# Kernel tuning notes

Hardware: AMD Instinct MI355X
Metric: run time of the kernel (lower is better)

Reference implementation:

```python
import jax, jax.numpy as jnp
import numpy as np

B, T, QD, KD, AD = 64, 2048, 512, 512, 512
SCALING = 1.0
NEG = -1e10


def setup_inputs() -> dict:
    key = jax.random.key(0)
    ks = jax.random.split(key, 10)
    s = 0.02
    return {
        "query": jax.random.normal(ks[0], (B, QD), jnp.float32),
        "keys": jax.random.normal(ks[1], (B, T, KD), jnp.float32),
        "value": jax.random.normal(ks[2], (B, T, KD), jnp.float32),
        "cover": jax.random.uniform(ks[3], (B, T), jnp.float32),
        "key_len": jax.random.randint(ks[4], (B,), T // 2, T + 1),
        "Wq": jax.random.normal(ks[5], (QD, AD), jnp.float32) * s,
        "bq": jnp.zeros((AD,), jnp.float32),
        "Wk": jax.random.normal(ks[6], (KD, AD), jnp.float32) * s,
        "Wc": jax.random.normal(ks[7], (1, AD), jnp.float32) * s,
        "Wo": jax.random.normal(ks[8], (AD, 1), jnp.float32) * s,
    }


def reference(query, keys, value, cover, key_len, Wq, bq, Wk, Wc, Wo):
    # projections
    q = query @ Wq + bq                      # [B, A]
    k = jnp.einsum("btd,da->bta", keys, Wk)  # [B, T, A]
    c = cover[..., None] * Wc[0]             # [B, T, A]  (Linear(1, A), no bias)
    # additive energy
    e = jnp.tanh(q[:, None, :] + k + c)      # [B, T, A]
    energy = jnp.einsum("bta,ao->bot", e, Wo)  # [B, 1, T]
    # mask padded positions (t >= key_len)
    mask = jnp.arange(T)[None, None, :] >= key_len[:, None, None]  # [B, 1, T]
    energy = jnp.where(mask, NEG, energy)
    attn = jax.nn.softmax(energy * SCALING, axis=2)  # [B, 1, T]
    context = jnp.einsum("bqt,btd->bqd", attn, value)[:, 0, :]  # [B, KD]
    return context, attn
```

## Files before the change

kernel.cpp:

```cpp
#include <hip/hip_runtime.h>
#include <hip/hip_bf16.h>

#define B_ 64
#define T_ 2048
#define D_ 512
#define A_ 512
#define BM 128
#define BN 128
#define BK 32
#define NSTEP (D_/BK)

typedef float f32x4_t __attribute__((ext_vector_type(4)));
typedef short bf16x8_t __attribute__((ext_vector_type(8)));

#define GLL16(g, l) __builtin_amdgcn_global_load_lds( \
    (const __attribute__((address_space(1))) void*)(g), \
    (__attribute__((address_space(3))) void*)(l), 16, 0, 0)

__global__ void __launch_bounds__(256) qproj_kernel(
    const float* __restrict__ query, const float* __restrict__ Wq,
    const float* __restrict__ bq, float* __restrict__ qbuf) {
  __shared__ float qs[D_];
  const int b = blockIdx.x, tid = threadIdx.x;
  qs[tid] = query[b*D_ + tid];
  qs[tid+256] = query[b*D_ + tid + 256];
  __syncthreads();
  float a0 = bq[tid], a1 = bq[tid+256];
  for (int d = 0; d < D_; ++d) {
    const float qv = qs[d];
    a0 += qv * Wq[d*A_ + tid];
    a1 += qv * Wq[d*A_ + tid + 256];
  }
  qbuf[b*A_ + tid] = a0;
  qbuf[b*A_ + tid+256] = a1;
}

__global__ void __launch_bounds__(256) wkprep_kernel(
    const float* __restrict__ Wk, unsigned int* __restrict__ slab) {
  __shared__ float tile[32][65];
  const int kb = blockIdx.x >> 3;
  const int a0 = (blockIdx.x & 7) * 64;
  const int tid = threadIdx.x;
  for (int p = 0; p < 8; ++p) {
    const int idx = p*256 + tid;
    const int k = idx >> 6, al = idx & 63;
    tile[k][al] = Wk[(kb*32 + k)*A_ + a0 + al];
  }
  __syncthreads();
  const int al = tid >> 2, c = tid & 3;
  const int a = a0 + al;
  union { __hip_bfloat162 h[2]; uint2 u; } w0, w1;
  w0.h[0] = __float22bfloat162_rn(make_float2(tile[c*8+0][al], tile[c*8+1][al]));
  w0.h[1] = __float22bfloat162_rn(make_float2(tile[c*8+2][al], tile[c*8+3][al]));
  w1.h[0] = __float22bfloat162_rn(make_float2(tile[c*8+4][al], tile[c*8+5][al]));
  w1.h[1] = __float22bfloat162_rn(make_float2(tile[c*8+6][al], tile[c*8+7][al]));
  const int cpos = c ^ ((a >> 1) & 3);
  *(uint4*)(slab + (kb*512 + a)*16 + cpos*4) =
      make_uint4(w0.u.x, w0.u.y, w1.u.x, w1.u.y);
}

__global__ void __launch_bounds__(256, 3) energy_kernel(
    const float* __restrict__ keys, const float* __restrict__ cover,
    const int* __restrict__ key_len, const unsigned char* __restrict__ slab,
    const float* __restrict__ qbuf, const float* __restrict__ Wc,
    const float* __restrict__ Wo, float* __restrict__ epart) {
  __shared__ __align__(16) float Afp[2][BM*BK];
  __shared__ __align__(16) unsigned char Bbuf[2][BN*64];
  __shared__ float redbuf[4][64];

  const int d = blockIdx.x;
  const int logical = (d & 7) * 512 + (d >> 3);
  const int ct = logical & 3;
  const int tt = (logical >> 2) & 15;
  const int b  = logical >> 6;

  const int t0 = tt * BM;
  const int kl = key_len[b];
  if (t0 >= kl) return;

  const int tid = threadIdx.x;
  const int wid = tid >> 6;
  const int lane = tid & 63;
  const int lq = lane >> 4, lr = lane & 15;
  const int wm = wid >> 1, wn = wid & 1;

  const int lrow = lane >> 3;
  const int lchunk = (lane & 7) ^ lrow;
  const float* agA[4];
  #pragma unroll
  for (int j = 0; j < 4; ++j) {
    const int r = (wid*4 + j)*8 + lrow;
    agA[j] = keys + ((size_t)b * T_ + t0 + r) * D_ + lchunk * 4;
  }
  const unsigned char* bsl = slab + ct * 8192 + wid * 1024 + lane * 16;

  f32x4_t acc[4][4];
  #pragma unroll
  for (int i = 0; i < 4; ++i)
    #pragma unroll
    for (int j = 0; j < 4; ++j) acc[i][j] = 0.0f;

  int b_off[4];
  #pragma unroll
  for (int nf = 0; nf < 4; ++nf) {
    const int r = wn*64 + nf*16 + lr;
    b_off[nf] = r*64 + ((lq ^ ((r >> 1) & 3)) << 4);
  }
  int a_off0[4], a_off1[4];
  #pragma unroll
  for (int mf = 0; mf < 4; ++mf) {
    const int r = wm*64 + mf*16 + lr;
    a_off0[mf] = r*BK + (((lq*2 + 0) ^ (r & 7)) << 2);
    a_off1[mf] = r*BK + (((lq*2 + 1) ^ (r & 7)) << 2);
  }

  {
    #pragma unroll
    for (int j = 0; j < 4; ++j)
      GLL16(agA[j], &Afp[0][(wid*4 + j)*256]);
    GLL16(bsl,        &Bbuf[0][wid*1024]);
    GLL16(bsl + 4096, &Bbuf[0][4096 + wid*1024]);
  }
  __syncthreads();

  for (int ks = 0; ks < NSTEP; ++ks) {
    const int cur = ks & 1;
    if (ks + 1 < NSTEP) {
      #pragma unroll
      for (int j = 0; j < 4; ++j)
        GLL16(agA[j] + (ks+1)*BK, &Afp[cur^1][(wid*4 + j)*256]);
      const unsigned char* g = bsl + (size_t)(ks+1)*32768;
      GLL16(g,        &Bbuf[cur^1][wid*1024]);
      GLL16(g + 4096, &Bbuf[cur^1][4096 + wid*1024]);
    }
    bf16x8_t aF[4], bF[4];
    #pragma unroll
    for (int mf = 0; mf < 4; ++mf) {
      const f32x4_t lo = *(const f32x4_t*)(&Afp[cur][a_off0[mf]]);
      const f32x4_t hi = *(const f32x4_t*)(&Afp[cur][a_off1[mf]]);
      union { __hip_bfloat162 h[4]; bf16x8_t v; } pk;
      pk.h[0] = __float22bfloat162_rn(make_float2(lo[0], lo[1]));
      pk.h[1] = __float22bfloat162_rn(make_float2(lo[2], lo[3]));
      pk.h[2] = __float22bfloat162_rn(make_float2(hi[0], hi[1]));
      pk.h[3] = __float22bfloat162_rn(make_float2(hi[2], hi[3]));
      aF[mf] = pk.v;
    }
    #pragma unroll
    for (int nf = 0; nf < 4; ++nf) bF[nf] = *(const bf16x8_t*)(&Bbuf[cur][b_off[nf]]);
    #pragma unroll
    for (int mf = 0; mf < 4; ++mf)
      #pragma unroll
      for (int nf = 0; nf < 4; ++nf)
        acc[mf][nf] = __builtin_amdgcn_mfma_f32_16x16x32_bf16(aF[mf], bF[nf], acc[mf][nf], 0, 0, 0);
    __syncthreads();
  }

  float cov[4][4];
  #pragma unroll
  for (int mf = 0; mf < 4; ++mf)
    #pragma unroll
    for (int j = 0; j < 4; ++j)
      cov[mf][j] = cover[(size_t)b*T_ + t0 + wm*64 + mf*16 + lq*4 + j];

  float ep[4][4];
  #pragma unroll
  for (int mf = 0; mf < 4; ++mf)
    #pragma unroll
    for (int j = 0; j < 4; ++j) ep[mf][j] = 0.f;

  #pragma unroll
  for (int nf = 0; nf < 4; ++nf) {
    const int n = ct*BN + wn*64 + nf*16 + lr;
    const float qv = qbuf[b*A_ + n];
    const float wc = Wc[n];
    const float wo = Wo[n];
    #pragma unroll
    for (int mf = 0; mf < 4; ++mf)
      #pragma unroll
      for (int j = 0; j < 4; ++j) {
        float p = acc[mf][nf][j] + qv + cov[mf][j] * wc;
        p = fminf(fmaxf(p, -15.f), 15.f);
        const float t2 = __expf(2.f * p);
        ep[mf][j] += wo * ((t2 - 1.f) * __builtin_amdgcn_rcpf(t2 + 1.f));
      }
  }
  #pragma unroll
  for (int mf = 0; mf < 4; ++mf)
    #pragma unroll
    for (int j = 0; j < 4; ++j) {
      float v = ep[mf][j];
      v += __shfl_xor(v, 1); v += __shfl_xor(v, 2);
      v += __shfl_xor(v, 4); v += __shfl_xor(v, 8);
      ep[mf][j] = v;
    }
  if (lr == 0) {
    #pragma unroll
    for (int mf = 0; mf < 4; ++mf)
      #pragma unroll
      for (int j = 0; j < 4; ++j)
        redbuf[wid][mf*16 + lq*4 + j] = ep[mf][j];
  }
  __syncthreads();
  if (tid < BM) {
    const int wmm = tid >> 6, rl = tid & 63;
    epart[((size_t)ct*B_ + b)*T_ + t0 + tid] = redbuf[wmm*2][rl] + redbuf[wmm*2+1][rl];
  }
}

__global__ void __launch_bounds__(1024) softmax_kernel(
    const float* __restrict__ epart, const int* __restrict__ key_len,
    float* __restrict__ attn) {
  __shared__ float sredM[16];
  __shared__ float sredS[16];
  const int b = blockIdx.x, tid = threadIdx.x;
  const int kl = key_len[b];
  float e0 = -3.0e38f, e1 = -3.0e38f;
  if (tid < kl)
    e0 = epart[(size_t)b*T_ + tid] + epart[((size_t)B_ + b)*T_ + tid]
       + epart[((size_t)2*B_ + b)*T_ + tid] + epart[((size_t)3*B_ + b)*T_ + tid];
  if (tid + 1024 < kl)
    e1 = epart[(size_t)b*T_ + tid+1024] + epart[((size_t)B_ + b)*T_ + tid+1024]
       + epart[((size_t)2*B_ + b)*T_ + tid+1024] + epart[((size_t)3*B_ + b)*T_ + tid+1024];
  float m = fmaxf(e0, e1);
  for (int s = 32; s; s >>= 1) m = fmaxf(m, __shfl_xor(m, s));
  if ((tid & 63) == 0) sredM[tid >> 6] = m;
  __syncthreads();
  float M = -3.0e38f;
  #pragma unroll
  for (int i = 0; i < 16; ++i) M = fmaxf(M, sredM[i]);
  const float p0 = (tid < kl) ? __expf(e0 - M) : 0.f;
  const float p1 = (tid + 1024 < kl) ? __expf(e1 - M) : 0.f;
  float s = p0 + p1;
  for (int k = 32; k; k >>= 1) s += __shfl_xor(s, k);
  if ((tid & 63) == 0) sredS[tid >> 6] = s;
  __syncthreads();
  float S = 0.f;
  #pragma unroll
  for (int i = 0; i < 16; ++i) S += sredS[i];
  const float inv = 1.f / S;
  attn[b*T_ + tid] = p0 * inv;
  attn[b*T_ + tid + 1024] = p1 * inv;
}

__global__ void __launch_bounds__(256) ctxpart_kernel(
    const float* __restrict__ value, const float* __restrict__ attn,
    const int* __restrict__ key_len, float* __restrict__ partial) {
  __shared__ float att_s[256];
  const int b = blockIdx.y, ch = blockIdx.x;
  const int tid = threadIdx.x;
  const int kl = key_len[b];
  const int tstart = ch * 256;
  const int tend = min(256, kl - tstart);
  float ax = 0.f, ay = 0.f;
  if (tend > 0) {
    att_s[tid] = attn[b*T_ + tstart + tid];
    __syncthreads();
    const float2* vp = (const float2*)(value + ((size_t)b*T_ + tstart)*D_) + tid;
    #pragma unroll 4
    for (int i = 0; i < tend; ++i) {
      const float w = att_s[i];
      const float2 v = vp[(size_t)i * 256];
      ax += w * v.x; ay += w * v.y;
    }
  }
  float2* pp = (float2*)(partial + (size_t)(b*8 + ch)*D_) + tid;
  *pp = make_float2(ax, ay);
}

__global__ void __launch_bounds__(256) ctxsum_kernel(
    const float* __restrict__ partial, float* __restrict__ ctx) {
  const int b = blockIdx.x, tid = threadIdx.x;
  float sx = 0.f, sy = 0.f;
  #pragma unroll
  for (int c = 0; c < 8; ++c) {
    const float2 v = *((const float2*)(partial + (size_t)(b*8 + c)*D_) + tid);
    sx += v.x; sy += v.y;
  }
  *((float2*)(ctx + (size_t)b*D_) + tid) = make_float2(sx, sy);
}

extern "C" void kernel_launch(void* const* d_in, const int* in_sizes, int n_in,
                              void* d_out, int out_size, void* d_ws, size_t ws_size,
                              hipStream_t stream) {
  const float* query  = (const float*)d_in[0];
  const float* keys   = (const float*)d_in[1];
  const float* value  = (const float*)d_in[2];
  const float* cover  = (const float*)d_in[3];
  const int*   key_len= (const int*)d_in[4];
  const float* Wq     = (const float*)d_in[5];
  const float* bq     = (const float*)d_in[6];
  const float* Wk     = (const float*)d_in[7];
  const float* Wc     = (const float*)d_in[8];
  const float* Wo     = (const float*)d_in[9];

  float* out = (float*)d_out;
  float* ctx_out  = out;
  float* attn_out = out + B_*A_;

  float* ws = (float*)d_ws;
  float* qbuf    = ws;
  float* epart   = ws + 32768;
  float* partial = ws + 32768 + 524288;
  unsigned int* slab = (unsigned int*)(ws + 32768 + 524288 + 262144);

  qproj_kernel<<<B_, 256, 0, stream>>>(query, Wq, bq, qbuf);
  wkprep_kernel<<<128, 256, 0, stream>>>(Wk, slab);
  energy_kernel<<<B_*(T_/BM)*(A_/BN), 256, 0, stream>>>(
      keys, cover, key_len, (const unsigned char*)slab, qbuf, Wc, Wo, epart);
  softmax_kernel<<<B_, 1024, 0, stream>>>(epart, key_len, attn_out);
  ctxpart_kernel<<<dim3(8, B_), 256, 0, stream>>>(value, attn_out, key_len, partial);
  ctxsum_kernel<<<B_, 256, 0, stream>>>(partial, ctx_out);
}
```

Before: 233.4 us.

## Load GEMM operands directly into registers instead of LDS staging

Replaces the LDS double-buffered global_load_lds pipeline in the energy GEMM with direct global-to-register loads. Each wave loads its own A (fp32 keys) and B (bf16 Wk slab) fragments and uses a register double buffer with a two-step unrolled loop. The block-level barriers are gone, and the LDS swizzle in the slab layout is dropped to match. In exchange, fragments shared by the two waves in each row or column are now fetched redundantly from global/L2. Register pressure also rises, which can hurt occupancy under the 3-block launch bound.

```diff
diff --git a/kernel.cpp b/kernel.cpp
--- a/kernel.cpp
+++ b/kernel.cpp
@@ -12,10 +12,6 @@
 
 typedef float f32x4_t __attribute__((ext_vector_type(4)));
 typedef short bf16x8_t __attribute__((ext_vector_type(8)));
-
-#define GLL16(g, l) __builtin_amdgcn_global_load_lds( \
-    (const __attribute__((address_space(1))) void*)(g), \
-    (__attribute__((address_space(3))) void*)(l), 16, 0, 0)
 
 __global__ void __launch_bounds__(256) qproj_kernel(
     const float* __restrict__ query, const float* __restrict__ Wq,
@@ -54,8 +50,7 @@
   w0.h[1] = __float22bfloat162_rn(make_float2(tile[c*8+2][al], tile[c*8+3][al]));
   w1.h[0] = __float22bfloat162_rn(make_float2(tile[c*8+4][al], tile[c*8+5][al]));
   w1.h[1] = __float22bfloat162_rn(make_float2(tile[c*8+6][al], tile[c*8+7][al]));
-  const int cpos = c ^ ((a >> 1) & 3);
-  *(uint4*)(slab + (kb*512 + a)*16 + cpos*4) =
+  *(uint4*)(slab + (kb*512 + a)*16 + c*4) =
       make_uint4(w0.u.x, w0.u.y, w1.u.x, w1.u.y);
 }
 
@@ -64,8 +59,6 @@
     const int* __restrict__ key_len, const unsigned char* __restrict__ slab,
     const float* __restrict__ qbuf, const float* __restrict__ Wc,
     const float* __restrict__ Wo, float* __restrict__ epart) {
-  __shared__ __align__(16) float Afp[2][BM*BK];
-  __shared__ __align__(16) unsigned char Bbuf[2][BN*64];
   __shared__ float redbuf[4][64];
 
   const int d = blockIdx.x;
@@ -84,15 +77,8 @@
   const int lq = lane >> 4, lr = lane & 15;
   const int wm = wid >> 1, wn = wid & 1;
 
-  const int lrow = lane >> 3;
-  const int lchunk = (lane & 7) ^ lrow;
-  const float* agA[4];
-  #pragma unroll
-  for (int j = 0; j < 4; ++j) {
-    const int r = (wid*4 + j)*8 + lrow;
-    agA[j] = keys + ((size_t)b * T_ + t0 + r) * D_ + lchunk * 4;
-  }
-  const unsigned char* bsl = slab + ct * 8192 + wid * 1024 + lane * 16;
+  const float* akeys = keys + ((size_t)b * T_ + t0 + wm*64 + lr) * D_ + lq*8;
+  const unsigned char* bsl = slab + (size_t)(ct*BN + wn*64 + lr)*64 + lq*16;
 
   f32x4_t acc[4][4];
   #pragma unroll
@@ -100,60 +86,50 @@
     #pragma unroll
     for (int j = 0; j < 4; ++j) acc[i][j] = 0.0f;
 
-  int b_off[4];
-  #pragma unroll
-  for (int nf = 0; nf < 4; ++nf) {
-    const int r = wn*64 + nf*16 + lr;
-    b_off[nf] = r*64 + ((lq ^ ((r >> 1) & 3)) << 4);
-  }
-  int a_off0[4], a_off1[4];
-  #pragma unroll
-  for (int mf = 0; mf < 4; ++mf) {
-    const int r = wm*64 + mf*16 + lr;
-    a_off0[mf] = r*BK + (((lq*2 + 0) ^ (r & 7)) << 2);
-    a_off1[mf] = r*BK + (((lq*2 + 1) ^ (r & 7)) << 2);
-  }
-
-  {
-    #pragma unroll
-    for (int j = 0; j < 4; ++j)
-      GLL16(agA[j], &Afp[0][(wid*4 + j)*256]);
-    GLL16(bsl,        &Bbuf[0][wid*1024]);
-    GLL16(bsl + 4096, &Bbuf[0][4096 + wid*1024]);
-  }
-  __syncthreads();
-
-  for (int ks = 0; ks < NSTEP; ++ks) {
-    const int cur = ks & 1;
-    if (ks + 1 < NSTEP) {
-      #pragma unroll
-      for (int j = 0; j < 4; ++j)
-        GLL16(agA[j] + (ks+1)*BK, &Afp[cur^1][(wid*4 + j)*256]);
-      const unsigned char* g = bsl + (size_t)(ks+1)*32768;
-      GLL16(g,        &Bbuf[cur^1][wid*1024]);
-      GLL16(g + 4096, &Bbuf[cur^1][4096 + wid*1024]);
-    }
-    bf16x8_t aF[4], bF[4];
-    #pragma unroll
-    for (int mf = 0; mf < 4; ++mf) {
-      const f32x4_t lo = *(const f32x4_t*)(&Afp[cur][a_off0[mf]]);
-      const f32x4_t hi = *(const f32x4_t*)(&Afp[cur][a_off1[mf]]);
-      union { __hip_bfloat162 h[4]; bf16x8_t v; } pk;
-      pk.h[0] = __float22bfloat162_rn(make_float2(lo[0], lo[1]));
-      pk.h[1] = __float22bfloat162_rn(make_float2(lo[2], lo[3]));
-      pk.h[2] = __float22bfloat162_rn(make_float2(hi[0], hi[1]));
-      pk.h[3] = __float22bfloat162_rn(make_float2(hi[2], hi[3]));
-      aF[mf] = pk.v;
-    }
-    #pragma unroll
-    for (int nf = 0; nf < 4; ++nf) bF[nf] = *(const bf16x8_t*)(&Bbuf[cur][b_off[nf]]);
-    #pragma unroll
-    for (int mf = 0; mf < 4; ++mf)
-      #pragma unroll
-      for (int nf = 0; nf < 4; ++nf)
-        acc[mf][nf] = __builtin_amdgcn_mfma_f32_16x16x32_bf16(aF[mf], bF[nf], acc[mf][nf], 0, 0, 0);
-    __syncthreads();
-  }
+  f32x4_t a0lo[4], a0hi[4], a1lo[4], a1hi[4];
+  bf16x8_t b0[4], b1[4];
+
+#define LOAD_STEP(ALO, AHI, BF, KS) do {                                   \
+    _Pragma("unroll")                                                      \
+    for (int mf = 0; mf < 4; ++mf) {                                       \
+      const float* p_ = akeys + mf*16*D_ + (KS)*BK;                        \
+      ALO[mf] = *(const f32x4_t*)(p_);                                     \
+      AHI[mf] = *(const f32x4_t*)(p_ + 4);                                 \
+    }                                                                      \
+    _Pragma("unroll")                                                      \
+    for (int nf = 0; nf < 4; ++nf)                                         \
+      BF[nf] = *(const bf16x8_t*)(bsl + (size_t)(KS)*32768 + nf*1024);     \
+  } while (0)
+
+#define MFMA_STEP(ALO, AHI, BF) do {                                       \
+    _Pragma("unroll")                                                      \
+    for (int mf = 0; mf < 4; ++mf) {                                       \
+      union { __hip_bfloat162 h[4]; bf16x8_t v; } pk_;                     \
+      pk_.h[0] = __float22bfloat162_rn(make_float2(ALO[mf][0], ALO[mf][1])); \
+      pk_.h[1] = __float22bfloat162_rn(make_float2(ALO[mf][2], ALO[mf][3])); \
+      pk_.h[2] = __float22bfloat162_rn(make_float2(AHI[mf][0], AHI[mf][1])); \
+      pk_.h[3] = __float22bfloat162_rn(make_float2(AHI[mf][2], AHI[mf][3])); \
+      _Pragma("unroll")                                                    \
+      for (int nf = 0; nf < 4; ++nf)                                       \
+        acc[mf][nf] = __builtin_amdgcn_mfma_f32_16x16x32_bf16(             \
+            pk_.v, BF[nf], acc[mf][nf], 0, 0, 0);                          \
+    }                                                                      \
+  } while (0)
+
+  LOAD_STEP(a0lo, a0hi, b0, 0);
+  #pragma unroll 1
+  for (int ks = 0; ks + 2 < NSTEP; ks += 2) {
+    LOAD_STEP(a1lo, a1hi, b1, ks + 1);
+    MFMA_STEP(a0lo, a0hi, b0);
+    LOAD_STEP(a0lo, a0hi, b0, ks + 2);
+    MFMA_STEP(a1lo, a1hi, b1);
+  }
+  LOAD_STEP(a1lo, a1hi, b1, NSTEP - 1);
+  MFMA_STEP(a0lo, a0hi, b0);
+  MFMA_STEP(a1lo, a1hi, b1);
+
+#undef LOAD_STEP
+#undef MFMA_STEP
 
   float cov[4][4];
   #pragma unroll
```

New measurement: 346.8 us. 1.49x slower.

## Stage keys through registers as bf16 and triple-buffer LDS with prefetch depth two

Applied to the files above, without the earlier changes.

The keys tile is now loaded into registers, converted to bf16 once, and stored swizzled into LDS. Previously fp32 data was copied into LDS and every wave converted it on each read, with each element converted by two waves. LDS bytes per A tile are halved, which makes room for a three-slot ring for both A and B at the same total LDS size. The ring prefetches two k-steps ahead with hand-placed waitcnt and barriers instead of __syncthreads. This costs extra VGPRs for the staged loads, and the vmcnt handling for the asynchronous B loads is delicate.

```diff
diff --git a/kernel.cpp b/kernel.cpp
--- a/kernel.cpp
+++ b/kernel.cpp
@@ -64,8 +64,8 @@
     const int* __restrict__ key_len, const unsigned char* __restrict__ slab,
     const float* __restrict__ qbuf, const float* __restrict__ Wc,
     const float* __restrict__ Wo, float* __restrict__ epart) {
-  __shared__ __align__(16) float Afp[2][BM*BK];
-  __shared__ __align__(16) unsigned char Bbuf[2][BN*64];
+  __shared__ __align__(16) unsigned char Abuf[3][BM*64];
+  __shared__ __align__(16) unsigned char Bbuf[3][BN*64];
   __shared__ float redbuf[4][64];
 
   const int d = blockIdx.x;
@@ -84,15 +84,13 @@
   const int lq = lane >> 4, lr = lane & 15;
   const int wm = wid >> 1, wn = wid & 1;
 
-  const int lrow = lane >> 3;
-  const int lchunk = (lane & 7) ^ lrow;
-  const float* agA[4];
-  #pragma unroll
-  for (int j = 0; j < 4; ++j) {
-    const int r = (wid*4 + j)*8 + lrow;
-    agA[j] = keys + ((size_t)b * T_ + t0 + r) * D_ + lchunk * 4;
-  }
-  const unsigned char* bsl = slab + ct * 8192 + wid * 1024 + lane * 16;
+  const int sr = tid >> 1, sh = tid & 1;
+  const float* agp = keys + ((size_t)b*T_ + t0 + sr)*D_ + sh*16;
+  const int sx = (sr >> 1) & 3;
+  const int sw0 = sr*64 + (((2*sh + 0) ^ sx) << 4);
+  const int sw1 = sr*64 + (((2*sh + 1) ^ sx) << 4);
+
+  const unsigned char* bsl = slab + ct*8192 + wid*1024 + lane*16;
 
   f32x4_t acc[4][4];
   #pragma unroll
@@ -100,59 +98,83 @@
     #pragma unroll
     for (int j = 0; j < 4; ++j) acc[i][j] = 0.0f;
 
-  int b_off[4];
+  int a_off[4], b_off[4];
+  #pragma unroll
+  for (int mf = 0; mf < 4; ++mf) {
+    const int r = wm*64 + mf*16 + lr;
+    a_off[mf] = r*64 + ((lq ^ ((r >> 1) & 3)) << 4);
+  }
   #pragma unroll
   for (int nf = 0; nf < 4; ++nf) {
     const int r = wn*64 + nf*16 + lr;
     b_off[nf] = r*64 + ((lq ^ ((r >> 1) & 3)) << 4);
   }
-  int a_off0[4], a_off1[4];
-  #pragma unroll
-  for (int mf = 0; mf < 4; ++mf) {
-    const int r = wm*64 + mf*16 + lr;
-    a_off0[mf] = r*BK + (((lq*2 + 0) ^ (r & 7)) << 2);
-    a_off1[mf] = r*BK + (((lq*2 + 1) ^ (r & 7)) << 2);
-  }
-
-  {
-    #pragma unroll
-    for (int j = 0; j < 4; ++j)
-      GLL16(agA[j], &Afp[0][(wid*4 + j)*256]);
-    GLL16(bsl,        &Bbuf[0][wid*1024]);
-    GLL16(bsl + 4096, &Bbuf[0][4096 + wid*1024]);
-  }
-  __syncthreads();
+
+  f32x4_t pA[4];
+  auto agload = [&](int ksrc) {
+    const float* p = agp + ksrc*BK;
+    pA[0] = *(const f32x4_t*)(p);
+    pA[1] = *(const f32x4_t*)(p + 4);
+    pA[2] = *(const f32x4_t*)(p + 8);
+    pA[3] = *(const f32x4_t*)(p + 12);
+  };
+  auto bgll = [&](int ksrc, unsigned char* Bdst) {
+    const unsigned char* g = bsl + (size_t)ksrc*32768;
+    GLL16(g,        Bdst + wid*1024);
+    GLL16(g + 4096, Bdst + 4096 + wid*1024);
+  };
+  auto apack = [&](unsigned char* Adst) {
+    union { __hip_bfloat162 h[2]; uint2 u; } q0, q1;
+    q0.h[0] = __float22bfloat162_rn(make_float2(pA[0][0], pA[0][1]));
+    q0.h[1] = __float22bfloat162_rn(make_float2(pA[0][2], pA[0][3]));
+    q1.h[0] = __float22bfloat162_rn(make_float2(pA[1][0], pA[1][1]));
+    q1.h[1] = __float22bfloat162_rn(make_float2(pA[1][2], pA[1][3]));
+    *(uint4*)(Adst + sw0) = make_uint4(q0.u.x, q0.u.y, q1.u.x, q1.u.y);
+    q0.h[0] = __float22bfloat162_rn(make_float2(pA[2][0], pA[2][1]));
+    q0.h[1] = __float22bfloat162_rn(make_float2(pA[2][2], pA[2][3]));
+    q1.h[0] = __float22bfloat162_rn(make_float2(pA[3][0], pA[3][1]));
+    q1.h[1] = __float22bfloat162_rn(make_float2(pA[3][2], pA[3][3]));
+    *(uint4*)(Adst + sw1) = make_uint4(q0.u.x, q0.u.y, q1.u.x, q1.u.y);
+  };
+
+  unsigned char *Ar = Abuf[0], *An = Abuf[1], *Aw = Abuf[2];
+  unsigned char *Br = Bbuf[0], *Bn = Bbuf[1], *Bw = Bbuf[2];
+
+  agload(0); bgll(0, Br);
+  apack(Ar);
+  agload(1); bgll(1, Bn);
+  apack(An);
+  asm volatile("s_waitcnt lgkmcnt(0)" ::: "memory");
+  __builtin_amdgcn_s_barrier();
+  __builtin_amdgcn_sched_barrier(0);
 
   for (int ks = 0; ks < NSTEP; ++ks) {
-    const int cur = ks & 1;
-    if (ks + 1 < NSTEP) {
-      #pragma unroll
-      for (int j = 0; j < 4; ++j)
-        GLL16(agA[j] + (ks+1)*BK, &Afp[cur^1][(wid*4 + j)*256]);
-      const unsigned char* g = bsl + (size_t)(ks+1)*32768;
-      GLL16(g,        &Bbuf[cur^1][wid*1024]);
-      GLL16(g + 4096, &Bbuf[cur^1][4096 + wid*1024]);
+    const bool pre = (ks + 2 < NSTEP);
+    if (pre) {
+      agload(ks + 2);
+      bgll(ks + 2, Bw);
     }
     bf16x8_t aF[4], bF[4];
     #pragma unroll
-    for (int mf = 0; mf < 4; ++mf) {
-      const f32x4_t lo = *(const f32x4_t*)(&Afp[cur][a_off0[mf]]);
-      const f32x4_t hi = *(const f32x4_t*)(&Afp[cur][a_off1[mf]]);
-      union { __hip_bfloat162 h[4]; bf16x8_t v; } pk;
-      pk.h[0] = __float22bfloat162_rn(make_float2(lo[0], lo[1]));
-      pk.h[1] = __float22bfloat162_rn(make_float2(lo[2], lo[3]));
-      pk.h[2] = __float22bfloat162_rn(make_float2(hi[0], hi[1]));
-      pk.h[3] = __float22bfloat162_rn(make_float2(hi[2], hi[3]));
-      aF[mf] = pk.v;
-    }
-    #pragma unroll
-    for (int nf = 0; nf < 4; ++nf) bF[nf] = *(const bf16x8_t*)(&Bbuf[cur][b_off[nf]]);
+    for (int mf = 0; mf < 4; ++mf) aF[mf] = *(const bf16x8_t*)(Ar + a_off[mf]);
+    #pragma unroll
+    for (int nf = 0; nf < 4; ++nf) bF[nf] = *(const bf16x8_t*)(Br + b_off[nf]);
     #pragma unroll
     for (int mf = 0; mf < 4; ++mf)
       #pragma unroll
       for (int nf = 0; nf < 4; ++nf)
         acc[mf][nf] = __builtin_amdgcn_mfma_f32_16x16x32_bf16(aF[mf], bF[nf], acc[mf][nf], 0, 0, 0);
-    __syncthreads();
+    if (pre) apack(Aw);
+    if (ks + 1 < NSTEP) {
+      if (!pre)
+        asm volatile("s_waitcnt vmcnt(0)" ::: "memory");
+      asm volatile("s_waitcnt lgkmcnt(0)" ::: "memory");
+      __builtin_amdgcn_s_barrier();
+      __builtin_amdgcn_sched_barrier(0);
+    }
+    unsigned char* t;
+    t = Ar; Ar = An; An = Aw; Aw = t;
+    t = Br; Br = Bn; Bn = Bw; Bw = t;
   }
 
   float cov[4][4];
```

New measurement: 239.8 us. 1.03x slower.
